# Kernel optimization log

Hardware: AMD Instinct MI355X
Metric: run time of the kernel (lower is better)

Reference implementation:

```python
import jax, jax.numpy as jnp
import numpy as np

N, E, G, L = 50000, 800000, 512, 4
DIN, D = 128, 64


def setup_inputs() -> dict:
    key = jax.random.key(0)
    ks = jax.random.split(key, 32)
    s = 0.1  # weight scale
    inp = {
        "nodes_feat": jax.random.normal(ks[0], (N, DIN), jnp.float32),
        "edges_feat": jax.random.normal(ks[1], (E, 1), jnp.float32),
        "nodes_num_norm_sqrt": jax.random.uniform(ks[2], (N, 1), jnp.float32),
        "edges_num_norm_sqrt": jax.random.uniform(ks[3], (E, 1), jnp.float32),
        "W_h": jax.random.normal(ks[4], (DIN, D), jnp.float32) * s,
        "b_h": jax.random.normal(ks[5], (D,), jnp.float32) * s,
        "W_e": jax.random.normal(ks[6], (1, D), jnp.float32) * s,
        "b_e": jax.random.normal(ks[7], (D,), jnp.float32) * s,
        "Wa": jax.random.normal(ks[8], (L, D, D), jnp.float32) * s,
        "ba": jax.random.normal(ks[9], (L, D), jnp.float32) * s,
        "Wb": jax.random.normal(ks[10], (L, D, D), jnp.float32) * s,
        "bb": jax.random.normal(ks[11], (L, D), jnp.float32) * s,
        "Wc": jax.random.normal(ks[12], (L, D, D), jnp.float32) * s,
        "bc": jax.random.normal(ks[13], (L, D), jnp.float32) * s,
        "Wd": jax.random.normal(ks[14], (L, D, D), jnp.float32) * s,
        "bd": jax.random.normal(ks[15], (L, D), jnp.float32) * s,
        "We": jax.random.normal(ks[16], (L, D, D), jnp.float32) * s,
        "be": jax.random.normal(ks[17], (L, D), jnp.float32) * s,
        "gamma_h": jnp.ones((L, D), jnp.float32),
        "beta_h": jnp.zeros((L, D), jnp.float32),
        "gamma_e": jnp.ones((L, D), jnp.float32),
        "beta_e": jnp.zeros((L, D), jnp.float32),
        "edge_src": jax.random.randint(ks[18], (E,), 0, N, jnp.int32),
        "edge_dst": jax.random.randint(ks[19], (E,), 0, N, jnp.int32),
        "node_graph_ids": jnp.sort(jax.random.randint(ks[20], (N,), 0, G, jnp.int32)),
        "num_graphs": G,
    }
    return inp


def _bn(x, gamma, beta):
    # BatchNorm1d, training mode (biased batch statistics)
    mu = jnp.mean(x, axis=0)
    var = jnp.var(x, axis=0)
    return gamma * (x - mu) * jax.lax.rsqrt(var + 1e-5) + beta


def reference(nodes_feat, edges_feat, nodes_num_norm_sqrt, edges_num_norm_sqrt,
              W_h, b_h, W_e, b_e,
              Wa, ba, Wb, bb, Wc, bc, Wd, bd, We, be,
              gamma_h, beta_h, gamma_e, beta_e,
              edge_src, edge_dst, node_graph_ids, num_graphs):
    seg = jax.ops.segment_sum
    n_nodes = nodes_feat.shape[0]
    h = nodes_feat @ W_h + b_h          # [N, D]
    e = edges_feat @ W_e + b_e          # [E, D]
    for l in range(Wa.shape[0]):
        h_in, e_in = h, e
        Ah = h @ Wa[l] + ba[l]
        Bh = h @ Wb[l] + bb[l]
        Dh = h @ Wd[l] + bd[l]
        Eh = h @ We[l] + be[l]
        e_new = (e @ Wc[l] + bc[l]) + Dh[edge_src] + Eh[edge_dst]   # [E, D]
        sigma = jax.nn.sigmoid(e_new)
        num = seg(sigma * Bh[edge_src], edge_dst, num_segments=n_nodes)
        den = seg(sigma, edge_dst, num_segments=n_nodes)
        h_new = Ah + num / (den + 1e-6)
        h_new = h_new * nodes_num_norm_sqrt      # graph norm
        e_new = e_new * edges_num_norm_sqrt
        h_new = jax.nn.relu(_bn(h_new, gamma_h[l], beta_h[l]))
        e_new = jax.nn.relu(_bn(e_new, gamma_e[l], beta_e[l]))
        h = h_in + h_new                          # residual
        e = e_in + e_new
    # dgl.mean_nodes: segment mean of node features per graph
    ones = jnp.ones((n_nodes, 1), h.dtype)
    counts = seg(ones, node_graph_ids, num_segments=num_graphs)
    hg = seg(h, node_graph_ids, num_segments=num_graphs) / jnp.maximum(counts, 1.0)
    return hg
```

## Files before the change

kernel.cpp:

```cpp
#include <hip/hip_runtime.h>
#include <cstddef>

#define DIN 128
#define DD 64

typedef unsigned short bfu;
typedef __attribute__((ext_vector_type(8))) short bf16x8;
typedef __attribute__((ext_vector_type(4))) float f32x4;

static __device__ __forceinline__ float bf2f(bfu u) {
    union { unsigned int i; float f; } v; v.i = ((unsigned int)u) << 16; return v.f;
}
static __device__ __forceinline__ bfu f2bf(float f) {
    union { float f; unsigned int i; } v; v.f = f;
    unsigned int r = v.i + 0x7FFFu + ((v.i >> 16) & 1u);
    return (bfu)(r >> 16);
}
static __device__ __forceinline__ float4 bf4_to_f4(ushort4 u) {
    return make_float4(bf2f(u.x), bf2f(u.y), bf2f(u.z), bf2f(u.w));
}
static __device__ __forceinline__ ushort4 f4_to_bf4(float4 f) {
    ushort4 u; u.x = f2bf(f.x); u.y = f2bf(f.y); u.z = f2bf(f.z); u.w = f2bf(f.w); return u;
}
static __device__ __forceinline__ float sigmoidf_(float x) {
    return 1.0f / (1.0f + __expf(-x));
}

__global__ __launch_bounds__(256) void embed_h_v9(
    const float* __restrict__ x, const float* __restrict__ Wh,
    const float* __restrict__ bh, float* __restrict__ h, int N)
{
    __shared__ float w[DIN][DD];
    __shared__ float xs[32][DIN];
    for (int i = threadIdx.x; i < DIN * DD / 4; i += 256)
        ((float4*)w)[i] = ((const float4*)Wh)[i];
    int row0 = blockIdx.x * 32;
    for (int i = threadIdx.x; i < 32 * DIN / 4; i += 256) {
        int r = i >> 5, k = (i & 31) * 4;
        int row = row0 + r;
        float4 v = make_float4(0.f, 0.f, 0.f, 0.f);
        if (row < N) v = *(const float4*)(x + (size_t)row * DIN + k);
        *(float4*)(&xs[r][k]) = v;
    }
    __syncthreads();
    int rl = threadIdx.x >> 6;
    int c  = threadIdx.x & 63;
    float b = bh[c];
    for (int rr = 0; rr < 8; ++rr) {
        int r = rl * 8 + rr;
        int row = row0 + r;
        if (row >= N) break;
        float acc = b;
        #pragma unroll
        for (int k = 0; k < DIN; k += 4) {
            float4 xv = *(const float4*)(&xs[r][k]);
            acc += xv.x * w[k][c] + xv.y * w[k+1][c] + xv.z * w[k+2][c] + xv.w * w[k+3][c];
        }
        h[(size_t)row * DD + c] = acc;
    }
}

__global__ void csr_hist_v9(const int* __restrict__ dst, int* __restrict__ counts, int E)
{
    for (int i = blockIdx.x * blockDim.x + threadIdx.x; i < E; i += gridDim.x * blockDim.x)
        atomicAdd(&counts[dst[i]], 1);
}

__global__ void csr_scan_a_v9(const int* __restrict__ counts, int* __restrict__ part,
                              int M, int CH)
{
    __shared__ int sd[256];
    int b = blockIdx.x, t = threadIdx.x;
    int idx = b * CH + t;
    int v = (t < CH && idx < M) ? counts[idx] : 0;
    sd[t] = v; __syncthreads();
    for (int off = 128; off > 0; off >>= 1) {
        if (t < off) sd[t] += sd[t + off];
        __syncthreads();
    }
    if (t == 0) part[b] = sd[0];
}

__global__ void csr_scan_b_v9(int* __restrict__ part)
{
    __shared__ int sd[256];
    int t = threadIdx.x;
    int v = part[t];
    sd[t] = v; __syncthreads();
    for (int off = 1; off < 256; off <<= 1) {
        int u = (t >= off) ? sd[t - off] : 0;
        __syncthreads();
        sd[t] += u;
        __syncthreads();
    }
    part[t] = sd[t] - v;
}

__global__ void csr_scan_c_v9(const int* __restrict__ counts, const int* __restrict__ part,
                              int* __restrict__ offsets, int* __restrict__ cursor,
                              int M, int CH)
{
    __shared__ int sd[256];
    int b = blockIdx.x, t = threadIdx.x;
    int idx = b * CH + t;
    int v = (t < CH && idx < M) ? counts[idx] : 0;
    sd[t] = v; __syncthreads();
    for (int off = 1; off < 256; off <<= 1) {
        int u = (t >= off) ? sd[t - off] : 0;
        __syncthreads();
        sd[t] += u;
        __syncthreads();
    }
    int excl = sd[t] - v + part[b];
    if (t < CH && idx < M) { offsets[idx] = excl; cursor[idx] = excl; }
}

__global__ void csr_scatter_v9(const int* __restrict__ dst, int* __restrict__ cursor,
                               int* __restrict__ csr_eid, int E)
{
    for (int i = blockIdx.x * blockDim.x + threadIdx.x; i < E; i += gridDim.x * blockDim.x) {
        int p = atomicAdd(&cursor[dst[i]], 1);
        csr_eid[p] = i;
    }
}

__global__ void perm_build_v9(const int* __restrict__ csr_eid, const int* __restrict__ esrc,
                              const float* __restrict__ enorm,
                              unsigned short* __restrict__ src_p,
                              float* __restrict__ enorm_p, int E)
{
    for (int i = blockIdx.x * blockDim.x + threadIdx.x; i < E; i += gridDim.x * blockDim.x) {
        int eid = csr_eid[i];
        src_p[i] = (unsigned short)esrc[eid];
        enorm_p[i] = enorm[eid];
    }
}

__global__ __launch_bounds__(256) void embed_e_perm_v9(
    const float* __restrict__ ef, const float* __restrict__ We,
    const float* __restrict__ be, const int* __restrict__ csr_eid,
    bfu* __restrict__ e, int E)
{
    int c = (threadIdx.x & 15) * 4;
    float4 w = *(const float4*)(We + c);
    float4 b = *(const float4*)(be + c);
    int total = E * 16;
    int stride = gridDim.x * blockDim.x;
    for (int u = blockIdx.x * blockDim.x + threadIdx.x; u < total; u += stride) {
        int j = u >> 4;
        float f = ef[csr_eid[j]];
        float4 o;
        o.x = f * w.x + b.x; o.y = f * w.y + b.y;
        o.z = f * w.z + b.z; o.w = f * w.w + b.w;
        *(ushort4*)(e + (size_t)j * DD + c) = f4_to_bf4(o);
    }
}

__global__ __launch_bounds__(256) void node_mm4_v9(
    const float* __restrict__ h,
    const float* __restrict__ Wa, const float* __restrict__ ba,
    const float* __restrict__ Wb, const float* __restrict__ bbv,
    const float* __restrict__ Wd, const float* __restrict__ bd,
    const float* __restrict__ We, const float* __restrict__ be,
    float* __restrict__ hrawA, bfu* __restrict__ DBh, bfu* __restrict__ Eh, int N)
{
    __shared__ float hs[64][DD];
    int row0 = blockIdx.x * 64;
    for (int i = threadIdx.x; i < 64 * 16; i += 256) {
        int r = i >> 4, cc = (i & 15) * 4;
        int row = row0 + r;
        float4 v = make_float4(0.f, 0.f, 0.f, 0.f);
        if (row < N) v = *(const float4*)(h + (size_t)row * DD + cc);
        *(float4*)(&hs[r][cc]) = v;
    }
    __syncthreads();
    int m = threadIdx.x >> 6;
    int c = threadIdx.x & 63;
    const float* W    = (m == 0) ? Wa : (m == 1) ? Wb : (m == 2) ? Wd : We;
    const float* bias = (m == 0) ? ba : (m == 1) ? bbv : (m == 2) ? bd : be;
    float wcol[DD];
    #pragma unroll
    for (int k = 0; k < DD; ++k) wcol[k] = W[k * DD + c];
    float b = bias[c];
    int rmax = (N - row0 < 64) ? (N - row0) : 64;
    for (int r = 0; r < rmax; ++r) {
        float acc = b;
        #pragma unroll
        for (int k = 0; k < DD; k += 4) {
            float4 hv = *(const float4*)(&hs[r][k]);
            acc += hv.x * wcol[k] + hv.y * wcol[k+1] + hv.z * wcol[k+2] + hv.w * wcol[k+3];
        }
        size_t row = (size_t)(row0 + r);
        if (m == 0)      hrawA[row * DD + c] = acc;
        else if (m == 1) DBh[row * 128 + 2 * c + 1] = f2bf(acc);
        else if (m == 2) DBh[row * 128 + 2 * c] = f2bf(acc);
        else             Eh[row * DD + c] = f2bf(acc);
    }
}

__global__ __launch_bounds__(256) void ec_gemm_v9(
    bfu* __restrict__ e, bfu* __restrict__ ecs,
    const float* __restrict__ Wc, const float* __restrict__ bc,
    const float* __restrict__ bnAB,
    int apply, int store_e, int E)
{
    int l  = threadIdx.x & 63;
    int lr = l & 15;
    int ld = l >> 4;

    bf16x8 bfrag[4][2];
    #pragma unroll
    for (int ct = 0; ct < 4; ++ct)
        #pragma unroll
        for (int kh = 0; kh < 2; ++kh)
            #pragma unroll
            for (int j = 0; j < 8; ++j)
                bfrag[ct][kh][j] = (short)f2bf(Wc[(kh * 32 + 8 * ld + j) * DD + ct * 16 + lr]);

    float bcl[4];
    #pragma unroll
    for (int ct = 0; ct < 4; ++ct) bcl[ct] = bc[ct * 16 + lr];

    float A0[8], B0[8], A1[8], B1[8];
    if (apply) {
        #pragma unroll
        for (int j = 0; j < 8; ++j) {
            A0[j] = bnAB[8 * ld + j];
            B0[j] = bnAB[64 + 8 * ld + j];
            A1[j] = bnAB[32 + 8 * ld + j];
            B1[j] = bnAB[64 + 32 + 8 * ld + j];
        }
    }

    int wg = blockIdx.x * 4 + (threadIdx.x >> 6);
    int nw = gridDim.x * 4;
    for (int base = wg * 16; base < E; base += nw * 16) {
        int row = base + lr;
        bf16x8 a0 = {0, 0, 0, 0, 0, 0, 0, 0};
        bf16x8 a1 = {0, 0, 0, 0, 0, 0, 0, 0};
        if (row < E) {
            size_t off = (size_t)row * DD + 8 * ld;
            bf16x8 r0 = *(const bf16x8*)(e + off);
            bf16x8 r1 = *(const bf16x8*)(e + off + 32);
            if (apply) {
                bf16x8 s0 = *(const bf16x8*)(ecs + off);
                bf16x8 s1 = *(const bf16x8*)(ecs + off + 32);
                #pragma unroll
                for (int j = 0; j < 8; ++j) {
                    float v0 = bf2f((bfu)r0[j]) + fmaxf(A0[j] * bf2f((bfu)s0[j]) + B0[j], 0.f);
                    float v1 = bf2f((bfu)r1[j]) + fmaxf(A1[j] * bf2f((bfu)s1[j]) + B1[j], 0.f);
                    a0[j] = (short)f2bf(v0);
                    a1[j] = (short)f2bf(v1);
                }
                if (store_e) {
                    *(bf16x8*)(e + off) = a0;
                    *(bf16x8*)(e + off + 32) = a1;
                }
            } else {
                a0 = r0; a1 = r1;
            }
        }
        #pragma unroll
        for (int ct = 0; ct < 4; ++ct) {
            f32x4 acc = {0.f, 0.f, 0.f, 0.f};
            acc = __builtin_amdgcn_mfma_f32_16x16x32_bf16(a0, bfrag[ct][0], acc, 0, 0, 0);
            acc = __builtin_amdgcn_mfma_f32_16x16x32_bf16(a1, bfrag[ct][1], acc, 0, 0, 0);
            #pragma unroll
            for (int j = 0; j < 4; ++j) {
                int orow = base + 4 * ld + j;
                if (orow < E)
                    ecs[(size_t)orow * DD + ct * 16 + lr] = f2bf(acc[j] + bcl[ct]);
            }
        }
    }
}

__global__ __launch_bounds__(256) void fused_accum_v9(
    bfu* __restrict__ ecs, float* __restrict__ hrawA,
    const bfu* __restrict__ DBh, const bfu* __restrict__ Eh,
    const int* __restrict__ coffs, const unsigned short* __restrict__ src_p,
    const float* __restrict__ enorm_p, const float* __restrict__ nnorm,
    float* __restrict__ stats, int N, int store_es)
{
    __shared__ float red[4][4][DD];
    int wid = threadIdx.x >> 6;
    int c   = threadIdx.x & 63;
    float se0 = 0.f, se20 = 0.f, se1 = 0.f, se21 = 0.f;
    float sh = 0.f, sh2 = 0.f;

    int gw = blockIdx.x * 4 + wid;
    int gstride = gridDim.x * 4;
    for (int n = gw; n < N; n += gstride) {
        int j0 = coffs[n], j1 = coffs[n + 1];
        float ehv = bf2f(Eh[(size_t)n * DD + c]);
        float a = hrawA[(size_t)n * DD + c];
        float num0 = 0.f, den0 = 0.f, num1 = 0.f, den1 = 0.f;
        int j = j0;
        for (; j + 1 < j1; j += 2) {
            int s0 = src_p[j], s1 = src_p[j + 1];
            float en0 = enorm_p[j], en1 = enorm_p[j + 1];
            bfu ec0 = ecs[(size_t)j * DD + c];
            bfu ec1 = ecs[(size_t)(j + 1) * DD + c];
            ushort2 db0 = *(const ushort2*)(DBh + (size_t)s0 * 128 + 2 * c);
            ushort2 db1 = *(const ushort2*)(DBh + (size_t)s1 * 128 + 2 * c);
            float er0 = bf2f(ec0) + bf2f(db0.x) + ehv;
            float er1 = bf2f(ec1) + bf2f(db1.x) + ehv;
            float sg0 = sigmoidf_(er0);
            float sg1 = sigmoidf_(er1);
            num0 += sg0 * bf2f(db0.y); den0 += sg0;
            num1 += sg1 * bf2f(db1.y); den1 += sg1;
            float es0 = er0 * en0, es1 = er1 * en1;
            if (store_es) {
                ecs[(size_t)j * DD + c] = f2bf(es0);
                ecs[(size_t)(j + 1) * DD + c] = f2bf(es1);
            }
            se0 += es0; se20 += es0 * es0;
            se1 += es1; se21 += es1 * es1;
        }
        if (j < j1) {
            int s0 = src_p[j];
            float en0 = enorm_p[j];
            bfu ec0 = ecs[(size_t)j * DD + c];
            ushort2 db0 = *(const ushort2*)(DBh + (size_t)s0 * 128 + 2 * c);
            float er0 = bf2f(ec0) + bf2f(db0.x) + ehv;
            float sg0 = sigmoidf_(er0);
            num0 += sg0 * bf2f(db0.y); den0 += sg0;
            float es0 = er0 * en0;
            if (store_es) ecs[(size_t)j * DD + c] = f2bf(es0);
            se0 += es0; se20 += es0 * es0;
        }
        float x = (a + (num0 + num1) / ((den0 + den1) + 1e-6f)) * nnorm[n];
        hrawA[(size_t)n * DD + c] = x;
        sh += x; sh2 += x * x;
    }

    red[wid][0][c] = se0 + se1;  red[wid][1][c] = se20 + se21;
    red[wid][2][c] = sh;         red[wid][3][c] = sh2;
    __syncthreads();
    if (threadIdx.x < DD) {
        int t = threadIdx.x;
        float t0 = 0.f, t1 = 0.f, t2 = 0.f, t3 = 0.f;
        #pragma unroll
        for (int w = 0; w < 4; ++w) {
            t0 += red[w][0][t]; t1 += red[w][1][t];
            t2 += red[w][2][t]; t3 += red[w][3][t];
        }
        unsafeAtomicAdd(&stats[t], t0);
        unsafeAtomicAdd(&stats[DD + t], t1);
        unsafeAtomicAdd(&stats[2 * DD + t], t2);
        unsafeAtomicAdd(&stats[3 * DD + t], t3);
    }
}

__global__ void bn_fin2_v9(const float* __restrict__ stats, float Ecnt, float Ncnt,
                           const float* __restrict__ gamma_e, const float* __restrict__ beta_e,
                           const float* __restrict__ gamma_h, const float* __restrict__ beta_h,
                           float* __restrict__ bnAB)
{
    int t = threadIdx.x;
    if (t < DD) {
        float mu  = stats[t] / Ecnt;
        float var = stats[DD + t] / Ecnt - mu * mu;
        float A = gamma_e[t] * rsqrtf(var + 1e-5f);
        bnAB[t] = A;
        bnAB[DD + t] = beta_e[t] - A * mu;
    } else {
        int cc = t - DD;
        float mu  = stats[2 * DD + cc] / Ncnt;
        float var = stats[3 * DD + cc] / Ncnt - mu * mu;
        float A = gamma_h[cc] * rsqrtf(var + 1e-5f);
        bnAB[2 * DD + cc] = A;
        bnAB[3 * DD + cc] = beta_h[cc] - A * mu;
    }
}

__global__ __launch_bounds__(256) void node_apply_v9(
    const float* __restrict__ hrawA, const float* __restrict__ bnAB,
    float* __restrict__ h, int N)
{
    int cc = (threadIdx.x & 15) * 4;
    float4 A = *(const float4*)(bnAB + 2 * DD + cc);
    float4 B = *(const float4*)(bnAB + 3 * DD + cc);
    int total = N * 16;
    int stride = gridDim.x * blockDim.x;
    for (int u = blockIdx.x * blockDim.x + threadIdx.x; u < total; u += stride) {
        size_t off = ((size_t)(u >> 4)) * DD + ((u & 15) * 4);
        float4 x   = *(const float4*)(hrawA + off);
        float4 hin = *(const float4*)(h + off);
        float4 y;
        y.x = hin.x + fmaxf(A.x * x.x + B.x, 0.f);
        y.y = hin.y + fmaxf(A.y * x.y + B.y, 0.f);
        y.z = hin.z + fmaxf(A.z * x.z + B.z, 0.f);
        y.w = hin.w + fmaxf(A.w * x.w + B.w, 0.f);
        *(float4*)(h + off) = y;
    }
}

__global__ __launch_bounds__(256) void readout_v9(
    const float* __restrict__ h, const int* __restrict__ gid,
    float* __restrict__ hg, float* __restrict__ counts, int N)
{
    int total = N * 16;
    int stride = gridDim.x * blockDim.x;
    for (int u = blockIdx.x * blockDim.x + threadIdx.x; u < total; u += stride) {
        int n = u >> 4;
        int c = (u & 15) * 4;
        int g = gid[n];
        float4 x = *(const float4*)(h + (size_t)n * DD + c);
        float* p = hg + (size_t)g * DD + c;
        unsafeAtomicAdd(p + 0, x.x);
        unsafeAtomicAdd(p + 1, x.y);
        unsafeAtomicAdd(p + 2, x.z);
        unsafeAtomicAdd(p + 3, x.w);
        if ((u & 15) == 0) unsafeAtomicAdd(&counts[g], 1.0f);
    }
}

__global__ void readout_div_v9(const float* __restrict__ hg,
                               const float* __restrict__ counts,
                               float* __restrict__ out, int GD)
{
    int i = blockIdx.x * blockDim.x + threadIdx.x;
    if (i < GD) {
        int g = i >> 6;
        out[i] = hg[i] / fmaxf(counts[g], 1.0f);
    }
}

extern "C" void kernel_launch(void* const* d_in, const int* in_sizes, int n_in,
                              void* d_out, int out_size, void* d_ws, size_t ws_size,
                              hipStream_t stream)
{
    const float* nodes_feat = (const float*)d_in[0];
    const float* edges_feat = (const float*)d_in[1];
    const float* nnorm      = (const float*)d_in[2];
    const float* enorm      = (const float*)d_in[3];
    const float* W_h = (const float*)d_in[4];
    const float* b_h = (const float*)d_in[5];
    const float* W_e = (const float*)d_in[6];
    const float* b_e = (const float*)d_in[7];
    const float* Wa  = (const float*)d_in[8];
    const float* ba  = (const float*)d_in[9];
    const float* Wb_ = (const float*)d_in[10];
    const float* bb_ = (const float*)d_in[11];
    const float* Wc  = (const float*)d_in[12];
    const float* bc  = (const float*)d_in[13];
    const float* Wd  = (const float*)d_in[14];
    const float* bd  = (const float*)d_in[15];
    const float* We_ = (const float*)d_in[16];
    const float* be_ = (const float*)d_in[17];
    const float* gamma_h = (const float*)d_in[18];
    const float* beta_h  = (const float*)d_in[19];
    const float* gamma_e = (const float*)d_in[20];
    const float* beta_e  = (const float*)d_in[21];
    const int* esrc = (const int*)d_in[22];
    const int* edst = (const int*)d_in[23];
    const int* gid  = (const int*)d_in[24];

    const int N = in_sizes[0] / DIN;
    const int E = in_sizes[1];
    const int G = out_size / DD;
    const int L = in_sizes[8] / (DD * DD);

    float* f = (float*)d_ws;
    float* h       = f; f += (size_t)N * DD;
    float* hrawA   = f; f += (size_t)N * DD;
    float* stats   = f; f += 256;
    float* bnAB    = f; f += 256;
    float* hg      = f; f += (size_t)G * DD;
    float* gcnt    = f; f += G;
    int*   coffs   = (int*)f; f += (size_t)(N + 2);
    float* enorm_p = f; f += (size_t)E;
    unsigned short* src_p = (unsigned short*)f; f += (size_t)((E + 1) / 2);
    bfu* bp = (bfu*)f;
    bfu* DBh = bp; bp += (size_t)N * 128;
    bfu* Eh  = bp; bp += (size_t)N * DD;
    bfu* e_p = bp; bp += (size_t)E * DD;
    bfu* ecs = bp; bp += (size_t)E * DD;
    int* ccounts = (int*)ecs;
    int* ccursor = ccounts + (N + 1);
    int* cpart   = ccursor + (N + 1);
    int* csr_eid = cpart + 256;

    dim3 blk(256);

    hipMemsetAsync(hg, 0, ((size_t)G * DD + G) * sizeof(float), stream);
    hipMemsetAsync(ccounts, 0, (size_t)(N + 1) * sizeof(int), stream);

    embed_h_v9<<<(N + 31) / 32, blk, 0, stream>>>(nodes_feat, W_h, b_h, h, N);

    const int M  = N + 1;
    const int CH = (M + 255) / 256;
    csr_hist_v9<<<2048, blk, 0, stream>>>(edst, ccounts, E);
    csr_scan_a_v9<<<256, blk, 0, stream>>>(ccounts, cpart, M, CH);
    csr_scan_b_v9<<<1, blk, 0, stream>>>(cpart);
    csr_scan_c_v9<<<256, blk, 0, stream>>>(ccounts, cpart, coffs, ccursor, M, CH);
    csr_scatter_v9<<<2048, blk, 0, stream>>>(edst, ccursor, csr_eid, E);
    perm_build_v9<<<2048, blk, 0, stream>>>(csr_eid, esrc, enorm, src_p, enorm_p, E);
    embed_e_perm_v9<<<2048, blk, 0, stream>>>(edges_feat, W_e, b_e, csr_eid, e_p, E);

    for (int l = 0; l < L; ++l) {
        node_mm4_v9<<<(N + 63) / 64, blk, 0, stream>>>(
            h, Wa + (size_t)l * DD * DD, ba + (size_t)l * DD,
            Wb_ + (size_t)l * DD * DD, bb_ + (size_t)l * DD,
            Wd + (size_t)l * DD * DD, bd + (size_t)l * DD,
            We_ + (size_t)l * DD * DD, be_ + (size_t)l * DD,
            hrawA, DBh, Eh, N);
        hipMemsetAsync(stats, 0, 256 * sizeof(float), stream);
        ec_gemm_v9<<<2048, blk, 0, stream>>>(
            e_p, ecs, Wc + (size_t)l * DD * DD, bc + (size_t)l * DD,
            bnAB,
            (l > 0) ? 1 : 0,
            (l < L - 1) ? 1 : 0, E);
        fused_accum_v9<<<2048, blk, 0, stream>>>(
            ecs, hrawA, DBh, Eh,
            coffs, src_p, enorm_p, nnorm, stats, N,
            (l < L - 1) ? 1 : 0);
        bn_fin2_v9<<<1, 128, 0, stream>>>(
            stats, (float)E, (float)N,
            gamma_e + (size_t)l * DD, beta_e + (size_t)l * DD,
            gamma_h + (size_t)l * DD, beta_h + (size_t)l * DD, bnAB);
        node_apply_v9<<<1024, blk, 0, stream>>>(hrawA, bnAB, h, N);
    }

    readout_v9<<<1024, blk, 0, stream>>>(h, gid, hg, gcnt, N);
    readout_div_v9<<<(G * DD + 255) / 256, blk, 0, stream>>>(
        hg, gcnt, (float*)d_out, G * DD);
}
```

Measured before the change: 1.305 ms.

## Fuse edge GEMM into CSR accumulation and fold node BN-apply into next layer

The separate edge GEMM and per-node accumulation kernels become one kernel. Each wave walks a destination node's CSR edge range in 16-row MFMA tiles, computes the Wc projection, and immediately applies sigmoid, gated accumulation and edge-stat reduction. This removes the round trip of writing and rereading the Wc projection per layer. The node BN/ReLU/residual apply moves into the next layer's node matmul prologue, with only the final apply kept after the loop. The cost is ragged tiles: nodes with fewer than 16 edges waste MFMA lanes, and clamped rows add redundant loads.

```diff
diff --git a/kernel.cpp b/kernel.cpp
--- a/kernel.cpp
+++ b/kernel.cpp
@@ -26,7 +26,7 @@
     return 1.0f / (1.0f + __expf(-x));
 }
 
-__global__ __launch_bounds__(256) void embed_h_v9(
+__global__ __launch_bounds__(256) void embed_h_v10(
     const float* __restrict__ x, const float* __restrict__ Wh,
     const float* __restrict__ bh, float* __restrict__ h, int N)
 {
@@ -60,14 +60,14 @@
     }
 }
 
-__global__ void csr_hist_v9(const int* __restrict__ dst, int* __restrict__ counts, int E)
+__global__ void csr_hist_v10(const int* __restrict__ dst, int* __restrict__ counts, int E)
 {
     for (int i = blockIdx.x * blockDim.x + threadIdx.x; i < E; i += gridDim.x * blockDim.x)
         atomicAdd(&counts[dst[i]], 1);
 }
 
-__global__ void csr_scan_a_v9(const int* __restrict__ counts, int* __restrict__ part,
-                              int M, int CH)
+__global__ void csr_scan_a_v10(const int* __restrict__ counts, int* __restrict__ part,
+                               int M, int CH)
 {
     __shared__ int sd[256];
     int b = blockIdx.x, t = threadIdx.x;
@@ -81,7 +81,7 @@
     if (t == 0) part[b] = sd[0];
 }
 
-__global__ void csr_scan_b_v9(int* __restrict__ part)
+__global__ void csr_scan_b_v10(int* __restrict__ part)
 {
     __shared__ int sd[256];
     int t = threadIdx.x;
@@ -96,9 +96,9 @@
     part[t] = sd[t] - v;
 }
 
-__global__ void csr_scan_c_v9(const int* __restrict__ counts, const int* __restrict__ part,
-                              int* __restrict__ offsets, int* __restrict__ cursor,
-                              int M, int CH)
+__global__ void csr_scan_c_v10(const int* __restrict__ counts, const int* __restrict__ part,
+                               int* __restrict__ offsets, int* __restrict__ cursor,
+                               int M, int CH)
 {
     __shared__ int sd[256];
     int b = blockIdx.x, t = threadIdx.x;
@@ -115,8 +115,8 @@
     if (t < CH && idx < M) { offsets[idx] = excl; cursor[idx] = excl; }
 }
 
-__global__ void csr_scatter_v9(const int* __restrict__ dst, int* __restrict__ cursor,
-                               int* __restrict__ csr_eid, int E)
+__global__ void csr_scatter_v10(const int* __restrict__ dst, int* __restrict__ cursor,
+                                int* __restrict__ csr_eid, int E)
 {
     for (int i = blockIdx.x * blockDim.x + threadIdx.x; i < E; i += gridDim.x * blockDim.x) {
         int p = atomicAdd(&cursor[dst[i]], 1);
@@ -124,10 +124,10 @@
     }
 }
 
-__global__ void perm_build_v9(const int* __restrict__ csr_eid, const int* __restrict__ esrc,
-                              const float* __restrict__ enorm,
-                              unsigned short* __restrict__ src_p,
-                              float* __restrict__ enorm_p, int E)
+__global__ void perm_build_v10(const int* __restrict__ csr_eid, const int* __restrict__ esrc,
+                               const float* __restrict__ enorm,
+                               unsigned short* __restrict__ src_p,
+                               float* __restrict__ enorm_p, int E)
 {
     for (int i = blockIdx.x * blockDim.x + threadIdx.x; i < E; i += gridDim.x * blockDim.x) {
         int eid = csr_eid[i];
@@ -136,7 +136,7 @@
     }
 }
 
-__global__ __launch_bounds__(256) void embed_e_perm_v9(
+__global__ __launch_bounds__(256) void embed_e_perm_v10(
     const float* __restrict__ ef, const float* __restrict__ We,
     const float* __restrict__ be, const int* __restrict__ csr_eid,
     bfu* __restrict__ e, int E)
@@ -156,8 +156,9 @@
     }
 }
 
-__global__ __launch_bounds__(256) void node_mm4_v9(
-    const float* __restrict__ h,
+__global__ __launch_bounds__(256) void node_mm4_v10(
+    float* __restrict__ h, const float* __restrict__ hrawX,
+    const float* __restrict__ bnAB, int apply,
     const float* __restrict__ Wa, const float* __restrict__ ba,
     const float* __restrict__ Wb, const float* __restrict__ bbv,
     const float* __restrict__ Wd, const float* __restrict__ bd,
@@ -166,12 +167,31 @@
 {
     __shared__ float hs[64][DD];
     int row0 = blockIdx.x * 64;
-    for (int i = threadIdx.x; i < 64 * 16; i += 256) {
-        int r = i >> 4, cc = (i & 15) * 4;
-        int row = row0 + r;
-        float4 v = make_float4(0.f, 0.f, 0.f, 0.f);
-        if (row < N) v = *(const float4*)(h + (size_t)row * DD + cc);
-        *(float4*)(&hs[r][cc]) = v;
+    {
+        int cc4 = (threadIdx.x & 15) * 4;
+        float4 A = make_float4(0,0,0,0), B = A;
+        if (apply) {
+            A = *(const float4*)(bnAB + 2 * DD + cc4);
+            B = *(const float4*)(bnAB + 3 * DD + cc4);
+        }
+        for (int i = threadIdx.x; i < 64 * 16; i += 256) {
+            int r = i >> 4;
+            int row = row0 + r;
+            float4 v = make_float4(0.f, 0.f, 0.f, 0.f);
+            if (row < N) {
+                size_t off = (size_t)row * DD + cc4;
+                v = *(const float4*)(h + off);
+                if (apply) {
+                    float4 x = *(const float4*)(hrawX + off);
+                    v.x += fmaxf(A.x * x.x + B.x, 0.f);
+                    v.y += fmaxf(A.y * x.y + B.y, 0.f);
+                    v.z += fmaxf(A.z * x.z + B.z, 0.f);
+                    v.w += fmaxf(A.w * x.w + B.w, 0.f);
+                    *(float4*)(h + off) = v;
+                }
+            }
+            *(float4*)(&hs[r][cc4]) = v;
+        }
     }
     __syncthreads();
     int m = threadIdx.x >> 6;
@@ -198,13 +218,19 @@
     }
 }
 
-__global__ __launch_bounds__(256) void ec_gemm_v9(
-    bfu* __restrict__ e, bfu* __restrict__ ecs,
+__global__ __launch_bounds__(256) void edge_fused_v10(
+    bfu* __restrict__ e, bfu* __restrict__ es,
     const float* __restrict__ Wc, const float* __restrict__ bc,
     const float* __restrict__ bnAB,
-    int apply, int store_e, int E)
-{
+    float* __restrict__ hrawA,
+    const bfu* __restrict__ DBh, const bfu* __restrict__ Eh,
+    const int* __restrict__ coffs, const unsigned short* __restrict__ src_p,
+    const float* __restrict__ enorm_p, const float* __restrict__ nnorm,
+    float* __restrict__ stats, int N, int E, int apply, int store)
+{
+    __shared__ float red[4][4][DD];
     int l  = threadIdx.x & 63;
+    int wid = threadIdx.x >> 6;
     int lr = l & 15;
     int ld = l >> 4;
 
@@ -226,116 +252,116 @@
         #pragma unroll
         for (int j = 0; j < 8; ++j) {
             A0[j] = bnAB[8 * ld + j];
-            B0[j] = bnAB[64 + 8 * ld + j];
+            B0[j] = bnAB[DD + 8 * ld + j];
             A1[j] = bnAB[32 + 8 * ld + j];
-            B1[j] = bnAB[64 + 32 + 8 * ld + j];
-        }
-    }
-
-    int wg = blockIdx.x * 4 + (threadIdx.x >> 6);
-    int nw = gridDim.x * 4;
-    for (int base = wg * 16; base < E; base += nw * 16) {
-        int row = base + lr;
-        bf16x8 a0 = {0, 0, 0, 0, 0, 0, 0, 0};
-        bf16x8 a1 = {0, 0, 0, 0, 0, 0, 0, 0};
-        if (row < E) {
-            size_t off = (size_t)row * DD + 8 * ld;
-            bf16x8 r0 = *(const bf16x8*)(e + off);
-            bf16x8 r1 = *(const bf16x8*)(e + off + 32);
-            if (apply) {
-                bf16x8 s0 = *(const bf16x8*)(ecs + off);
-                bf16x8 s1 = *(const bf16x8*)(ecs + off + 32);
-                #pragma unroll
-                for (int j = 0; j < 8; ++j) {
-                    float v0 = bf2f((bfu)r0[j]) + fmaxf(A0[j] * bf2f((bfu)s0[j]) + B0[j], 0.f);
-                    float v1 = bf2f((bfu)r1[j]) + fmaxf(A1[j] * bf2f((bfu)s1[j]) + B1[j], 0.f);
-                    a0[j] = (short)f2bf(v0);
-                    a1[j] = (short)f2bf(v1);
-                }
-                if (store_e) {
-                    *(bf16x8*)(e + off) = a0;
-                    *(bf16x8*)(e + off + 32) = a1;
-                }
-            } else {
-                a0 = r0; a1 = r1;
-            }
-        }
-        #pragma unroll
-        for (int ct = 0; ct < 4; ++ct) {
-            f32x4 acc = {0.f, 0.f, 0.f, 0.f};
-            acc = __builtin_amdgcn_mfma_f32_16x16x32_bf16(a0, bfrag[ct][0], acc, 0, 0, 0);
-            acc = __builtin_amdgcn_mfma_f32_16x16x32_bf16(a1, bfrag[ct][1], acc, 0, 0, 0);
-            #pragma unroll
-            for (int j = 0; j < 4; ++j) {
-                int orow = base + 4 * ld + j;
-                if (orow < E)
-                    ecs[(size_t)orow * DD + ct * 16 + lr] = f2bf(acc[j] + bcl[ct]);
-            }
-        }
-    }
-}
-
-__global__ __launch_bounds__(256) void fused_accum_v9(
-    bfu* __restrict__ ecs, float* __restrict__ hrawA,
-    const bfu* __restrict__ DBh, const bfu* __restrict__ Eh,
-    const int* __restrict__ coffs, const unsigned short* __restrict__ src_p,
-    const float* __restrict__ enorm_p, const float* __restrict__ nnorm,
-    float* __restrict__ stats, int N, int store_es)
-{
-    __shared__ float red[4][4][DD];
-    int wid = threadIdx.x >> 6;
-    int c   = threadIdx.x & 63;
-    float se0 = 0.f, se20 = 0.f, se1 = 0.f, se21 = 0.f;
-    float sh = 0.f, sh2 = 0.f;
+            B1[j] = bnAB[DD + 32 + 8 * ld + j];
+        }
+    } else {
+        #pragma unroll
+        for (int j = 0; j < 8; ++j) { A0[j]=B0[j]=A1[j]=B1[j]=0.f; }
+    }
+
+    float se[4]  = {0.f,0.f,0.f,0.f}, se2[4] = {0.f,0.f,0.f,0.f};
+    float sh[4]  = {0.f,0.f,0.f,0.f}, sh2[4] = {0.f,0.f,0.f,0.f};
 
     int gw = blockIdx.x * 4 + wid;
     int gstride = gridDim.x * 4;
     for (int n = gw; n < N; n += gstride) {
         int j0 = coffs[n], j1 = coffs[n + 1];
-        float ehv = bf2f(Eh[(size_t)n * DD + c]);
-        float a = hrawA[(size_t)n * DD + c];
-        float num0 = 0.f, den0 = 0.f, num1 = 0.f, den1 = 0.f;
-        int j = j0;
-        for (; j + 1 < j1; j += 2) {
-            int s0 = src_p[j], s1 = src_p[j + 1];
-            float en0 = enorm_p[j], en1 = enorm_p[j + 1];
-            bfu ec0 = ecs[(size_t)j * DD + c];
-            bfu ec1 = ecs[(size_t)(j + 1) * DD + c];
-            ushort2 db0 = *(const ushort2*)(DBh + (size_t)s0 * 128 + 2 * c);
-            ushort2 db1 = *(const ushort2*)(DBh + (size_t)s1 * 128 + 2 * c);
-            float er0 = bf2f(ec0) + bf2f(db0.x) + ehv;
-            float er1 = bf2f(ec1) + bf2f(db1.x) + ehv;
-            float sg0 = sigmoidf_(er0);
-            float sg1 = sigmoidf_(er1);
-            num0 += sg0 * bf2f(db0.y); den0 += sg0;
-            num1 += sg1 * bf2f(db1.y); den1 += sg1;
-            float es0 = er0 * en0, es1 = er1 * en1;
-            if (store_es) {
-                ecs[(size_t)j * DD + c] = f2bf(es0);
-                ecs[(size_t)(j + 1) * DD + c] = f2bf(es1);
+        float num[4] = {0.f,0.f,0.f,0.f}, den[4] = {0.f,0.f,0.f,0.f};
+        float ehv[4];
+        #pragma unroll
+        for (int ct = 0; ct < 4; ++ct) ehv[ct] = bf2f(Eh[(size_t)n * DD + ct * 16 + lr]);
+
+        for (int jb = j0; jb < j1; jb += 16) {
+            int nvalid = j1 - jb;
+            int arow = jb + lr;
+            int lrow = (arow < E) ? arow : (E - 1);
+            size_t aoff = (size_t)lrow * DD + 8 * ld;
+            bf16x8 a0, a1;
+            {
+                bf16x8 r0 = *(const bf16x8*)(e + aoff);
+                bf16x8 r1 = *(const bf16x8*)(e + aoff + 32);
+                if (apply) {
+                    bf16x8 s0 = *(const bf16x8*)(es + aoff);
+                    bf16x8 s1 = *(const bf16x8*)(es + aoff + 32);
+                    #pragma unroll
+                    for (int j = 0; j < 8; ++j) {
+                        float v0 = bf2f((bfu)r0[j]) + fmaxf(A0[j] * bf2f((bfu)s0[j]) + B0[j], 0.f);
+                        float v1 = bf2f((bfu)r1[j]) + fmaxf(A1[j] * bf2f((bfu)s1[j]) + B1[j], 0.f);
+                        a0[j] = (short)f2bf(v0);
+                        a1[j] = (short)f2bf(v1);
+                    }
+                    if (store && lr < nvalid) {
+                        *(bf16x8*)(e + aoff) = a0;
+                        *(bf16x8*)(e + aoff + 32) = a1;
+                    }
+                } else {
+                    a0 = r0; a1 = r1;
+                }
             }
-            se0 += es0; se20 += es0 * es0;
-            se1 += es1; se21 += es1 * es1;
-        }
-        if (j < j1) {
-            int s0 = src_p[j];
-            float en0 = enorm_p[j];
-            bfu ec0 = ecs[(size_t)j * DD + c];
-            ushort2 db0 = *(const ushort2*)(DBh + (size_t)s0 * 128 + 2 * c);
-            float er0 = bf2f(ec0) + bf2f(db0.x) + ehv;
-            float sg0 = sigmoidf_(er0);
-            num0 += sg0 * bf2f(db0.y); den0 += sg0;
-            float es0 = er0 * en0;
-            if (store_es) ecs[(size_t)j * DD + c] = f2bf(es0);
-            se0 += es0; se20 += es0 * es0;
-        }
-        float x = (a + (num0 + num1) / ((den0 + den1) + 1e-6f)) * nnorm[n];
-        hrawA[(size_t)n * DD + c] = x;
-        sh += x; sh2 += x * x;
-    }
-
-    red[wid][0][c] = se0 + se1;  red[wid][1][c] = se20 + se21;
-    red[wid][2][c] = sh;         red[wid][3][c] = sh2;
+            float enr[4]; int sr[4]; bool vm[4];
+            #pragma unroll
+            for (int j = 0; j < 4; ++j) {
+                int rj = 4 * ld + j;
+                vm[j] = rj < nvalid;
+                int row = jb + (vm[j] ? rj : 0);
+                enr[j] = enorm_p[row];
+                sr[j]  = src_p[row];
+            }
+            #pragma unroll
+            for (int ct = 0; ct < 4; ++ct) {
+                f32x4 acc = {0.f, 0.f, 0.f, 0.f};
+                acc = __builtin_amdgcn_mfma_f32_16x16x32_bf16(a0, bfrag[ct][0], acc, 0, 0, 0);
+                acc = __builtin_amdgcn_mfma_f32_16x16x32_bf16(a1, bfrag[ct][1], acc, 0, 0, 0);
+                #pragma unroll
+                for (int j = 0; j < 4; ++j) {
+                    ushort2 db = *(const ushort2*)(DBh + (size_t)sr[j] * 128 + 2 * (ct * 16 + lr));
+                    float er = acc[j] + bcl[ct] + bf2f(db.x) + ehv[ct];
+                    float sg = sigmoidf_(er);
+                    float esv = er * enr[j];
+                    if (vm[j]) {
+                        num[ct] += sg * bf2f(db.y);
+                        den[ct] += sg;
+                        se[ct]  += esv;
+                        se2[ct] += esv * esv;
+                        if (store)
+                            es[(size_t)(jb + 4 * ld + j) * DD + ct * 16 + lr] = f2bf(esv);
+                    }
+                }
+            }
+        }
+        #pragma unroll
+        for (int ct = 0; ct < 4; ++ct) {
+            num[ct] += __shfl_xor(num[ct], 16); num[ct] += __shfl_xor(num[ct], 32);
+            den[ct] += __shfl_xor(den[ct], 16); den[ct] += __shfl_xor(den[ct], 32);
+        }
+        if (ld == 0) {
+            float nn = nnorm[n];
+            #pragma unroll
+            for (int ct = 0; ct < 4; ++ct) {
+                size_t off = (size_t)n * DD + ct * 16 + lr;
+                float x = (hrawA[off] + num[ct] / (den[ct] + 1e-6f)) * nn;
+                hrawA[off] = x;
+                sh[ct] += x; sh2[ct] += x * x;
+            }
+        }
+    }
+
+    #pragma unroll
+    for (int ct = 0; ct < 4; ++ct) {
+        se[ct]  += __shfl_xor(se[ct], 16);  se[ct]  += __shfl_xor(se[ct], 32);
+        se2[ct] += __shfl_xor(se2[ct], 16); se2[ct] += __shfl_xor(se2[ct], 32);
+    }
+    if (ld == 0) {
+        #pragma unroll
+        for (int ct = 0; ct < 4; ++ct) {
+            red[wid][0][ct * 16 + lr] = se[ct];
+            red[wid][1][ct * 16 + lr] = se2[ct];
+            red[wid][2][ct * 16 + lr] = sh[ct];
+            red[wid][3][ct * 16 + lr] = sh2[ct];
+        }
+    }
     __syncthreads();
     if (threadIdx.x < DD) {
         int t = threadIdx.x;
@@ -352,10 +378,10 @@
     }
 }
 
-__global__ void bn_fin2_v9(const float* __restrict__ stats, float Ecnt, float Ncnt,
-                           const float* __restrict__ gamma_e, const float* __restrict__ beta_e,
-                           const float* __restrict__ gamma_h, const float* __restrict__ beta_h,
-                           float* __restrict__ bnAB)
+__global__ void bn_fin2_v10(const float* __restrict__ stats, float Ecnt, float Ncnt,
+                            const float* __restrict__ gamma_e, const float* __restrict__ beta_e,
+                            const float* __restrict__ gamma_h, const float* __restrict__ beta_h,
+                            float* __restrict__ bnAB)
 {
     int t = threadIdx.x;
     if (t < DD) {
@@ -374,8 +400,8 @@
     }
 }
 
-__global__ __launch_bounds__(256) void node_apply_v9(
-    const float* __restrict__ hrawA, const float* __restrict__ bnAB,
+__global__ __launch_bounds__(256) void node_apply_v10(
+    const float* __restrict__ hrawX, const float* __restrict__ bnAB,
     float* __restrict__ h, int N)
 {
     int cc = (threadIdx.x & 15) * 4;
@@ -385,7 +411,7 @@
     int stride = gridDim.x * blockDim.x;
     for (int u = blockIdx.x * blockDim.x + threadIdx.x; u < total; u += stride) {
         size_t off = ((size_t)(u >> 4)) * DD + ((u & 15) * 4);
-        float4 x   = *(const float4*)(hrawA + off);
+        float4 x   = *(const float4*)(hrawX + off);
         float4 hin = *(const float4*)(h + off);
         float4 y;
         y.x = hin.x + fmaxf(A.x * x.x + B.x, 0.f);
@@ -396,7 +422,7 @@
     }
 }
 
-__global__ __launch_bounds__(256) void readout_v9(
+__global__ __launch_bounds__(256) void readout_v10(
     const float* __restrict__ h, const int* __restrict__ gid,
     float* __restrict__ hg, float* __restrict__ counts, int N)
 {
@@ -416,9 +442,9 @@
     }
 }
 
-__global__ void readout_div_v9(const float* __restrict__ hg,
-                               const float* __restrict__ counts,
-                               float* __restrict__ out, int GD)
+__global__ void readout_div_v10(const float* __restrict__ hg,
+                                const float* __restrict__ counts,
+                                float* __restrict__ out, int GD)
 {
     int i = blockIdx.x * blockDim.x + threadIdx.x;
     if (i < GD) {
@@ -476,8 +502,8 @@
     bfu* DBh = bp; bp += (size_t)N * 128;
     bfu* Eh  = bp; bp += (size_t)N * DD;
     bfu* e_p = bp; bp += (size_t)E * DD;
-    bfu* ecs = bp; bp += (size_t)E * DD;
-    int* ccounts = (int*)ecs;
+    bfu* es  = bp; bp += (size_t)E * DD;
+    int* ccounts = (int*)es;
     int* ccursor = ccounts + (N + 1);
     int* cpart   = ccursor + (N + 1);
     int* csr_eid = cpart + 256;
@@ -487,43 +513,41 @@
     hipMemsetAsync(hg, 0, ((size_t)G * DD + G) * sizeof(float), stream);
     hipMemsetAsync(ccounts, 0, (size_t)(N + 1) * sizeof(int), stream);
 
-    embed_h_v9<<<(N + 31) / 32, blk, 0, stream>>>(nodes_feat, W_h, b_h, h, N);
+    embed_h_v10<<<(N + 31) / 32, blk, 0, stream>>>(nodes_feat, W_h, b_h, h, N);
 
     const int M  = N + 1;
     const int CH = (M + 255) / 256;
-    csr_hist_v9<<<2048, blk, 0, stream>>>(edst, ccounts, E);
-    csr_scan_a_v9<<<256, blk, 0, stream>>>(ccounts, cpart, M, CH);
-    csr_scan_b_v9<<<1, blk, 0, stream>>>(cpart);
-    csr_scan_c_v9<<<256, blk, 0, stream>>>(ccounts, cpart, coffs, ccursor, M, CH);
-    csr_scatter_v9<<<2048, blk, 0, stream>>>(edst, ccursor, csr_eid, E);
-    perm_build_v9<<<2048, blk, 0, stream>>>(csr_eid, esrc, enorm, src_p, enorm_p, E);
-    embed_e_perm_v9<<<2048, blk, 0, stream>>>(edges_feat, W_e, b_e, csr_eid, e_p, E);
+    csr_hist_v10<<<2048, blk, 0, stream>>>(edst, ccounts, E);
+    csr_scan_a_v10<<<256, blk, 0, stream>>>(ccounts, cpart, M, CH);
+    csr_scan_b_v10<<<1, blk, 0, stream>>>(cpart);
+    csr_scan_c_v10<<<256, blk, 0, stream>>>(ccounts, cpart, coffs, ccursor, M, CH);
+    csr_scatter_v10<<<2048, blk, 0, stream>>>(edst, ccursor, csr_eid, E);
+    perm_build_v10<<<2048, blk, 0, stream>>>(csr_eid, esrc, enorm, src_p, enorm_p, E);
+    embed_e_perm_v10<<<2048, blk, 0, stream>>>(edges_feat, W_e, b_e, csr_eid, e_p, E);
 
     for (int l = 0; l < L; ++l) {
-        node_mm4_v9<<<(N + 63) / 64, blk, 0, stream>>>(
-            h, Wa + (size_t)l * DD * DD, ba + (size_t)l * DD,
+        node_mm4_v10<<<(N + 63) / 64, blk, 0, stream>>>(
+            h, hrawA, bnAB, (l > 0) ? 1 : 0,
+            Wa + (size_t)l * DD * DD, ba + (size_t)l * DD,
             Wb_ + (size_t)l * DD * DD, bb_ + (size_t)l * DD,
             Wd + (size_t)l * DD * DD, bd + (size_t)l * DD,
             We_ + (size_t)l * DD * DD, be_ + (size_t)l * DD,
             hrawA, DBh, Eh, N);
         hipMemsetAsync(stats, 0, 256 * sizeof(float), stream);
-        ec_gemm_v9<<<2048, blk, 0, stream>>>(
-            e_p, ecs, Wc + (size_t)l * DD * DD, bc + (size_t)l * DD,
-            bnAB,
+        edge_fused_v10<<<2048, blk, 0, stream>>>(
+            e_p, es, Wc + (size_t)l * DD * DD, bc + (size_t)l * DD,
+            bnAB, hrawA, DBh, Eh,
+            coffs, src_p, enorm_p, nnorm, stats, N, E,
             (l > 0) ? 1 : 0,
-            (l < L - 1) ? 1 : 0, E);
-        fused_accum_v9<<<2048, blk, 0, stream>>>(
-            ecs, hrawA, DBh, Eh,
-            coffs, src_p, enorm_p, nnorm, stats, N,
             (l < L - 1) ? 1 : 0);
-        bn_fin2_v9<<<1, 128, 0, stream>>>(
+        bn_fin2_v10<<<1, 128, 0, stream>>>(
             stats, (float)E, (float)N,
             gamma_e + (size_t)l * DD, beta_e + (size_t)l * DD,
             gamma_h + (size_t)l * DD, beta_h + (size_t)l * DD, bnAB);
-        node_apply_v9<<<1024, blk, 0, stream>>>(hrawA, bnAB, h, N);
-    }
-
-    readout_v9<<<1024, blk, 0, stream>>>(h, gid, hg, gcnt, N);
-    readout_div_v9<<<(G * DD + 255) / 256, blk, 0, stream>>>(
+    }
+
+    node_apply_v10<<<1024, blk, 0, stream>>>(hrawA, bnAB, h, N);
+    readout_v10<<<1024, blk, 0, stream>>>(h, gid, hg, gcnt, N);
+    readout_div_v10<<<(G * DD + 255) / 256, blk, 0, stream>>>(
         hg, gcnt, (float*)d_out, G * DD);
 }
```

Result: slower. 2.188 ms (+67.6%).
